# Optimization experiments

Measured on AMD Instinct MI355X. Metric: run time of the kernel, lower is better.

Reference implementation:

```python
import jax, jax.numpy as jnp
import numpy as np

B, S, E = 2, 4096, 1024
H = 16
W = 256  # attention_window == chunk size; attn width = 3*W


def _chunk3(x):
    # x: [b, nc, w, h, d] -> stack (prev, cur, next) chunks on last axis: [b, nc, w, h, d, 3]
    prev = jnp.pad(x[:, :-1], ((0, 0), (1, 0), (0, 0), (0, 0), (0, 0)))
    nxt = jnp.pad(x[:, 1:], ((0, 0), (0, 1), (0, 0), (0, 0), (0, 0)))
    return jnp.stack([prev, x, nxt], axis=-1)


def setup_inputs() -> dict:
    key = jax.random.key(0)
    ks = jax.random.split(key, 4)
    hs = jax.random.normal(ks[0], (B, S, E), jnp.float32)

    def lin(k):
        kw, kb = jax.random.split(k)
        return (jax.random.normal(kw, (E, E), jnp.float32) * 0.02,
                jax.random.normal(kb, (E,), jnp.float32) * 0.02)

    Wq, bq = lin(ks[1])
    Wk, bk = lin(ks[2])
    Wv, bv = lin(ks[3])
    return {"hidden_states": hs, "Wq": Wq, "bq": bq, "Wk": Wk, "bk": bk, "Wv": Wv, "bv": bv}


def reference(hidden_states, Wq, bq, Wk, bk, Wv, bv):
    b, s, e = hidden_states.shape
    h, w = H, W
    d = e // h
    nc = s // w  # number of non-overlapping chunks

    # torch nn.Linear: y = x @ W.T + b ; q scaled by 1/sqrt(head_dim)
    q = (hidden_states @ Wq.T + bq) * (1.0 / np.sqrt(d))
    k = hidden_states @ Wk.T + bk
    v = hidden_states @ Wv.T + bv
    q = q.reshape(b, s, h, d)
    k = k.reshape(b, s, h, d)
    v = v.reshape(b, s, h, d)

    # ---- sliding_chunks_no_overlap_matmul_qk ----
    cq = q.reshape(b, nc, w, h, d)
    ck3 = _chunk3(k.reshape(b, nc, w, h, d))  # [b,nc,w,h,d,3]
    # [b,nc,w,h,3,w] -> [b,s,h,3w]
    scores = jnp.einsum('bcxhd,bcyhde->bcxhey', cq, ck3).reshape(b, s, h, 3 * w)

    # ---- mask_invalid_locations (same math as Longformer's helper) ----
    ii = jnp.arange(w)[:, None]
    cc = jnp.arange(w + 1)[None, :]
    beg_mask = cc < (w - ii)   # [w, w+1] applied to first w rows, first w+1 cols
    end_mask = cc >= (w - ii)  # flipped mask, last w rows, last w+1 cols
    neg_inf = jnp.array(-jnp.inf, scores.dtype)
    beg = jnp.where(beg_mask[None, :, None, :], neg_inf, scores[:, :w, :, :w + 1])
    scores = scores.at[:, :w, :, :w + 1].set(beg)
    end = jnp.where(end_mask[None, :, None, :], neg_inf, scores[:, s - w:, :, 3 * w - (w + 1):])
    scores = scores.at[:, s - w:, :, 3 * w - (w + 1):].set(end)

    # softmax in float32 (as in original), cast back
    probs = jax.nn.softmax(scores.astype(jnp.float32), axis=-1).astype(hidden_states.dtype)

    # ---- sliding_chunks_no_overlap_matmul_pv ----
    cp = probs.reshape(b, nc, w, h, 3, w)          # bcwhpd (d = key pos in chunk)
    cv3 = _chunk3(v.reshape(b, nc, w, h, d))       # bcdhep (d = pos, e = head_dim, p = 3)
    attn = jnp.einsum('bcwhpd,bcdhep->bcwhe', cp, cv3).reshape(b, s, h, d)

    return attn.reshape(b, s, e)
```

## Files before the change

### kernel.cpp

```cpp
#include <hip/hip_runtime.h>
#include <math.h>

#define BB  2
#define SS  4096
#define EE  1024
#define HH  16
#define DD  64
#define WW  256
#define NCC 16
#define MTOT (BB*SS)

typedef __attribute__((ext_vector_type(4))) float f32x4;
typedef __attribute__((ext_vector_type(8))) short bf16x8;

__device__ __forceinline__ void gl_lds16(const void* g, void* l) {
  __builtin_amdgcn_global_load_lds(
      (const __attribute__((address_space(1))) unsigned int*)g,
      (__attribute__((address_space(3))) unsigned int*)l,
      16, 0, 0);
}

__device__ __forceinline__ unsigned bf16rne(float f) {
  unsigned u = __float_as_uint(f);
  return (u + (((u >> 16) & 1u) + 0x7fffu)) >> 16;
}

__device__ __forceinline__ unsigned long long pack64(unsigned a, unsigned b,
                                                     unsigned c2, unsigned d) {
  return (unsigned long long)(a | (b << 16)) |
         ((unsigned long long)(c2 | (d << 16)) << 32);
}

__global__ __launch_bounds__(256) void split_kernel(
    const float* __restrict__ x, unsigned short* __restrict__ hi,
    unsigned short* __restrict__ lo)
{
  const size_t i = (size_t)blockIdx.x * 256 + threadIdx.x;
  const float4 v = ((const float4*)x)[i];
  float f[4] = {v.x, v.y, v.z, v.w};
  unsigned short h[4], l[4];
  #pragma unroll
  for (int j = 0; j < 4; ++j) {
    unsigned u  = __float_as_uint(f[j]);
    unsigned uh = u & 0xFFFF0000u;
    h[j] = (unsigned short)(uh >> 16);
    float r = f[j] - __uint_as_float(uh);
    unsigned ur = __float_as_uint(r);
    ur += ((ur >> 16) & 1u) + 0x7FFFu;
    l[j] = (unsigned short)(ur >> 16);
  }
  *(ushort4*)&hi[4*i] = make_ushort4(h[0], h[1], h[2], h[3]);
  *(ushort4*)&lo[4*i] = make_ushort4(l[0], l[1], l[2], l[3]);
}

struct ProjArgs {
  const unsigned short* Wh;
  const unsigned short* Wl;
  const float* bias;
  unsigned short* outHi;
  unsigned short* outLo;
  float scale;
};

__global__ __launch_bounds__(256) void mfma_proj(
    const unsigned short* __restrict__ Ahi,
    const unsigned short* __restrict__ Alo,
    ProjArgs p0, ProjArgs p1, ProjArgs p2)
{
  __shared__ __align__(16) unsigned short lds[4][4096];
  const int tid  = threadIdx.x;
  const int lane = tid & 63;
  const int wid  = tid >> 6;
  const int wr   = wid >> 1, wc = wid & 1;
  const int m0   = blockIdx.x * 128, n0 = blockIdx.y * 128;
  const ProjArgs P = (blockIdx.z == 0) ? p0 : ((blockIdx.z == 1) ? p1 : p2);

  const int q0 = tid, q1 = 256 + tid;
  const int row0 = ((q0 >> 5) << 3) | (q0 & 7), kc0 = (q0 >> 3) & 3;
  const int row1 = ((q1 >> 5) << 3) | (q1 & 7), kc1 = (q1 >> 3) & 3;

  const size_t aoff0 = (size_t)(m0 + row0) * 2048 + (size_t)(kc0 * 16);
  const size_t aoff1 = (size_t)(m0 + row1) * 2048 + (size_t)(kc1 * 16);
  const size_t boff0 = (size_t)(n0 + row0) * 2048 + (size_t)(kc0 * 16);
  const size_t boff1 = (size_t)(n0 + row1) * 2048 + (size_t)(kc1 * 16);

  const int dst0 = (wid * 64) * 16;
  const int dst1 = (256 + wid * 64) * 16;

  const char* gAh = (const char*)Ahi;
  const char* gAl = (const char*)Alo;
  const char* gBh = (const char*)P.Wh;
  const char* gBl = (const char*)P.Wl;

  const int fr = lane & 15;
  const int kc = lane >> 4;
  int a_o[4], b_o[4];
  #pragma unroll
  for (int f = 0; f < 4; ++f) {
    int r = wr * 64 + f * 16 + fr;
    a_o[f] = ((r >> 3) << 9) | (kc << 7) | ((r & 7) << 4);
    r = wc * 64 + f * 16 + fr;
    b_o[f] = ((r >> 3) << 9) | (kc << 7) | ((r & 7) << 4);
  }

  f32x4 acc[4][4];
  #pragma unroll
  for (int i = 0; i < 4; ++i)
    #pragma unroll
    for (int j = 0; j < 4; ++j) acc[i][j] = (f32x4){0.f, 0.f, 0.f, 0.f};

  char* L0 = (char*)&lds[0][0];
  char* L1 = (char*)&lds[1][0];
  char* L2 = (char*)&lds[2][0];
  char* L3 = (char*)&lds[3][0];

  for (int ks = 0; ks < 32; ++ks) {
    const size_t kb = (size_t)ks * 64;
    __syncthreads();
    gl_lds16(gAh + aoff0 + kb, L0 + dst0);
    gl_lds16(gAh + aoff1 + kb, L0 + dst1);
    gl_lds16(gAl + aoff0 + kb, L1 + dst0);
    gl_lds16(gAl + aoff1 + kb, L1 + dst1);
    gl_lds16(gBh + boff0 + kb, L2 + dst0);
    gl_lds16(gBh + boff1 + kb, L2 + dst1);
    gl_lds16(gBl + boff0 + kb, L3 + dst0);
    gl_lds16(gBl + boff1 + kb, L3 + dst1);
    __syncthreads();

    bf16x8 ah[4], al[4], bh[4], bl[4];
    #pragma unroll
    for (int f = 0; f < 4; ++f) {
      ah[f] = *(const bf16x8*)(L0 + a_o[f]);
      al[f] = *(const bf16x8*)(L1 + a_o[f]);
      bh[f] = *(const bf16x8*)(L2 + b_o[f]);
      bl[f] = *(const bf16x8*)(L3 + b_o[f]);
    }
    #pragma unroll
    for (int i = 0; i < 4; ++i)
      #pragma unroll
      for (int j = 0; j < 4; ++j)
        acc[i][j] = __builtin_amdgcn_mfma_f32_16x16x32_bf16(ah[i], bh[j], acc[i][j], 0, 0, 0);
    #pragma unroll
    for (int i = 0; i < 4; ++i)
      #pragma unroll
      for (int j = 0; j < 4; ++j)
        acc[i][j] = __builtin_amdgcn_mfma_f32_16x16x32_bf16(ah[i], bl[j], acc[i][j], 0, 0, 0);
    #pragma unroll
    for (int i = 0; i < 4; ++i)
      #pragma unroll
      for (int j = 0; j < 4; ++j)
        acc[i][j] = __builtin_amdgcn_mfma_f32_16x16x32_bf16(al[i], bh[j], acc[i][j], 0, 0, 0);
  }

  const int r4 = (lane >> 4) << 2;
  #pragma unroll
  for (int j = 0; j < 4; ++j) {
    const int col = n0 + wc * 64 + j * 16 + fr;
    const float bv = P.bias[col];
    #pragma unroll
    for (int i = 0; i < 4; ++i) {
      const int rrow = m0 + wr * 64 + i * 16 + r4;
      #pragma unroll
      for (int v = 0; v < 4; ++v) {
        const float val = (acc[i][j][v] + bv) * P.scale;
        const unsigned u = __float_as_uint(val);
        const float r = val - __uint_as_float(u & 0xFFFF0000u);
        unsigned ur = __float_as_uint(r);
        ur += ((ur >> 16) & 1u) + 0x7FFFu;
        const size_t o = (size_t)(rrow + v) * EE + col;
        P.outHi[o] = (unsigned short)(u >> 16);
        P.outLo[o] = (unsigned short)(ur >> 16);
      }
    }
  }
}

__global__ __launch_bounds__(256, 2) void attn_mfma(
    const unsigned short* __restrict__ Qh_g, const unsigned short* __restrict__ Ql_g,
    const unsigned short* __restrict__ Kh_g, const unsigned short* __restrict__ Kl_g,
    const unsigned short* __restrict__ Vh_g, const unsigned short* __restrict__ Vl_g,
    float* __restrict__ Og)
{
  __shared__ __align__(16) unsigned short Kf[2][2048];
  __shared__ __align__(16) unsigned short Vt[2][2048];
  __shared__ unsigned long long Pscr[4][256];

  const int c = blockIdx.x, h = blockIdx.y, b = blockIdx.z;
  const int tid = threadIdx.x;
  const int lane = tid & 63, wid = tid >> 6;
  const int g = lane >> 4, lq = lane & 15;

  const size_t qrow0 = (size_t)(b * NCC + c) * WW;
  const int colh = h * DD;

  bf16x8 qfh[4][2], qfl[4][2];
  #pragma unroll
  for (int s = 0; s < 4; ++s)
    #pragma unroll
    for (int ch = 0; ch < 2; ++ch) {
      const size_t off = (qrow0 + wid*64 + s*16 + lq) * EE + colh + ch*32 + g*8;
      qfh[s][ch] = *(const bf16x8*)(Qh_g + off);
      qfl[s][ch] = *(const bf16x8*)(Ql_g + off);
    }

  f32x4 Oa[4][4];
  #pragma unroll
  for (int i = 0; i < 4; ++i)
    #pragma unroll
    for (int j = 0; j < 4; ++j) Oa[i][j] = (f32x4){0.f, 0.f, 0.f, 0.f};
  float m[4], lsum[4];
  #pragma unroll
  for (int s = 0; s < 4; ++s) { m[s] = -1e30f; lsum[s] = 0.f; }

  const int kK = 16*(wid & 1) + lq;
  const int dK = 32*(wid >> 1) + g*8;
  const int stv = tid >> 5, idxv = tid & 31;
  const int kV = 16*(stv >> 2) + (idxv >> 1);
  const int dV = 16*(stv & 3) + 8*(idxv & 1);
  const int C0  = ((dV >> 4) << 6) | ((kV >> 3) << 4) | (dV & 15);
  const int swW = (((dV >> 4) & 1) << 2) | (((kV >> 3) & 1) << 1) | ((dV >> 3) & 1);
  const int vel = kV & 7;

  const long krow0_base = (long)qrow0 - WW;
  const int t0 = (c == 0) ? 8 : 0;
  const int tN = (c == NCC-1) ? 16 : 24;

  uint4 rkh, rkl, rvh, rvl;
  {
    const long kr = krow0_base + (long)t0*32;
    const size_t offK = (size_t)(kr + kK) * EE + colh + dK;
    const size_t offV = (size_t)(kr + kV) * EE + colh + dV;
    rkh = *(const uint4*)(Kh_g + offK); rkl = *(const uint4*)(Kl_g + offK);
    rvh = *(const uint4*)(Vh_g + offV); rvl = *(const uint4*)(Vl_g + offV);
  }

  for (int tt = t0; tt < tN; ++tt) {
    __syncthreads();
    *(uint4*)&Kf[0][wid*512 + lane*8] = rkh;
    *(uint4*)&Kf[1][wid*512 + lane*8] = rkl;
    {
      const unsigned hw[4] = {rvh.x, rvh.y, rvh.z, rvh.w};
      const unsigned lw[4] = {rvl.x, rvl.y, rvl.z, rvl.w};
      #pragma unroll
      for (int t = 0; t < 8; ++t) {
        const int ii = C0*8 + ((t ^ swW) << 3) + vel;
        Vt[0][ii] = (unsigned short)(hw[t >> 1] >> ((t & 1) * 16));
        Vt[1][ii] = (unsigned short)(lw[t >> 1] >> ((t & 1) * 16));
      }
    }
    __syncthreads();

    if (tt + 1 < tN) {
      const long kr = krow0_base + (long)(tt+1)*32;
      const size_t offK = (size_t)(kr + kK) * EE + colh + dK;
      const size_t offV = (size_t)(kr + kV) * EE + colh + dV;
      rkh = *(const uint4*)(Kh_g + offK); rkl = *(const uint4*)(Kl_g + offK);
      rvh = *(const uint4*)(Vh_g + offV); rvl = *(const uint4*)(Vl_g + offV);
    }

    bf16x8 kfh[2][2], kfl[2][2];
    #pragma unroll
    for (int f = 0; f < 4; ++f) {
      const int o = f*512 + lane*8;
      kfh[f & 1][f >> 1] = *(const bf16x8*)&Kf[0][o];
      kfl[f & 1][f >> 1] = *(const bf16x8*)&Kf[1][o];
    }

    bf16x8 vfh[4], vfl[4];
    #pragma unroll
    for (int ds = 0; ds < 4; ++ds) {
      const int rch = ds*64 + g*16 + lq;
      const int rsw = (((rch >> 6) & 1) << 2) | (((rch >> 4) & 1) << 1) | ((rch >> 3) & 1);
      vfh[ds] = *(const bf16x8*)&Vt[0][(rch ^ rsw) * 8];
      vfl[ds] = *(const bf16x8*)&Vt[1][(rch ^ rsw) * 8];
    }

    #pragma unroll
    for (int s = 0; s < 4; ++s) {
      f32x4 ac0 = (f32x4){0.f,0.f,0.f,0.f}, ac1 = (f32x4){0.f,0.f,0.f,0.f};
      #pragma unroll
      for (int ch = 0; ch < 2; ++ch) {
        ac0 = __builtin_amdgcn_mfma_f32_16x16x32_bf16(kfh[0][ch], qfh[s][ch], ac0, 0,0,0);
        ac0 = __builtin_amdgcn_mfma_f32_16x16x32_bf16(kfh[0][ch], qfl[s][ch], ac0, 0,0,0);
        ac0 = __builtin_amdgcn_mfma_f32_16x16x32_bf16(kfl[0][ch], qfh[s][ch], ac0, 0,0,0);
        ac1 = __builtin_amdgcn_mfma_f32_16x16x32_bf16(kfh[1][ch], qfh[s][ch], ac1, 0,0,0);
        ac1 = __builtin_amdgcn_mfma_f32_16x16x32_bf16(kfh[1][ch], qfl[s][ch], ac1, 0,0,0);
        ac1 = __builtin_amdgcn_mfma_f32_16x16x32_bf16(kfl[1][ch], qfh[s][ch], ac1, 0,0,0);
      }

      float tmax = fmaxf(fmaxf(fmaxf(ac0[0],ac0[1]), fmaxf(ac0[2],ac0[3])),
                         fmaxf(fmaxf(ac1[0],ac1[1]), fmaxf(ac1[2],ac1[3])));
      tmax = fmaxf(tmax, __shfl_xor(tmax, 16));
      tmax = fmaxf(tmax, __shfl_xor(tmax, 32));
      const float mo = m[s];
      const float mn = fmaxf(mo, tmax);
      m[s] = mn;
      const float sc = __expf(mo - mn);
      float pv[8];
      #pragma unroll
      for (int r = 0; r < 4; ++r) { pv[r] = __expf(ac0[r] - mn); pv[4+r] = __expf(ac1[r] - mn); }
      float ps = 0.f;
      #pragma unroll
      for (int r = 0; r < 8; ++r) ps += pv[r];
      lsum[s] = lsum[s] * sc + ps;
      #pragma unroll
      for (int ds = 0; ds < 4; ++ds) Oa[ds][s] *= sc;

      unsigned hb[8], lb[8];
      #pragma unroll
      for (int r = 0; r < 8; ++r) {
        hb[r] = bf16rne(pv[r]);
        const float rr = pv[r] - __uint_as_float(hb[r] << 16);
        lb[r] = bf16rne(rr);
      }
      const int pq = (g >> 1)*32 + lq*2 + (g & 1);
      Pscr[wid][pq]            = pack64(hb[0],hb[1],hb[2],hb[3]);
      Pscr[wid][pq + 64]       = pack64(hb[4],hb[5],hb[6],hb[7]);
      Pscr[wid][128 + pq]      = pack64(lb[0],lb[1],lb[2],lb[3]);
      Pscr[wid][128 + pq + 64] = pack64(lb[4],lb[5],lb[6],lb[7]);
      asm volatile("" ::: "memory");
      union U8 { unsigned long long q[2]; bf16x8 v; };
      U8 uh, ul;
      uh.q[0] = Pscr[wid][lane*2];       uh.q[1] = Pscr[wid][lane*2 + 1];
      ul.q[0] = Pscr[wid][128 + lane*2]; ul.q[1] = Pscr[wid][128 + lane*2 + 1];
      const bf16x8 pbh = uh.v;
      const bf16x8 pbl = ul.v;

      #pragma unroll
      for (int ds = 0; ds < 4; ++ds) {
        Oa[ds][s] = __builtin_amdgcn_mfma_f32_16x16x32_bf16(vfh[ds], pbh, Oa[ds][s], 0,0,0);
        Oa[ds][s] = __builtin_amdgcn_mfma_f32_16x16x32_bf16(vfl[ds], pbh, Oa[ds][s], 0,0,0);
        Oa[ds][s] = __builtin_amdgcn_mfma_f32_16x16x32_bf16(vfh[ds], pbl, Oa[ds][s], 0,0,0);
      }
    }
  }

  #pragma unroll
  for (int s = 0; s < 4; ++s) {
    float ls = lsum[s];
    ls += __shfl_xor(ls, 16);
    ls += __shfl_xor(ls, 32);
    const int x = wid*64 + s*16 + lq;
    const float nz = (c == 0) ? (float)x
                   : ((c == NCC-1) ? (float)(WW - 1 - x) : 0.f);
    ls += nz * __expf(0.f - m[s]);
    const float inv = 1.f / ls;
    float* op = Og + (qrow0 + x) * EE + colh;
    #pragma unroll
    for (int ds = 0; ds < 4; ++ds) {
      float4 r;
      r.x = Oa[ds][s][0]*inv; r.y = Oa[ds][s][1]*inv;
      r.z = Oa[ds][s][2]*inv; r.w = Oa[ds][s][3]*inv;
      *(float4*)(op + ds*16 + g*4) = r;
    }
  }
}

extern "C" void kernel_launch(void* const* d_in, const int* in_sizes, int n_in,
                              void* d_out, int out_size, void* d_ws, size_t ws_size,
                              hipStream_t stream) {
    const float* hs = (const float*)d_in[0];
    const float* Wq = (const float*)d_in[1];
    const float* bq = (const float*)d_in[2];
    const float* Wk = (const float*)d_in[3];
    const float* bk = (const float*)d_in[4];
    const float* Wv = (const float*)d_in[5];
    const float* bv = (const float*)d_in[6];
    float* out = (float*)d_out;

    const size_t mat  = (size_t)MTOT * EE;
    const size_t wmat = (size_t)EE * EE;

    unsigned short* w = (unsigned short*)d_ws;
    unsigned short* Ahi = w;            unsigned short* Alo = Ahi + mat;
    unsigned short* Wqh = Alo + mat;    unsigned short* Wql = Wqh + wmat;
    unsigned short* Wkh = Wql + wmat;   unsigned short* Wkl = Wkh + wmat;
    unsigned short* Wvh = Wkl + wmat;   unsigned short* Wvl = Wvh + wmat;
    unsigned short* Qhb = Wvl + wmat;   unsigned short* Qlb = Qhb + mat;
    unsigned short* Khb = Qlb + mat;    unsigned short* Klb = Khb + mat;
    unsigned short* Vhb = Klb + mat;    unsigned short* Vlb = Vhb + mat;

    split_kernel<<<(mat/4)/256,  256, 0, stream>>>(hs, Ahi, Alo);
    split_kernel<<<(wmat/4)/256, 256, 0, stream>>>(Wq, Wqh, Wql);
    split_kernel<<<(wmat/4)/256, 256, 0, stream>>>(Wk, Wkh, Wkl);
    split_kernel<<<(wmat/4)/256, 256, 0, stream>>>(Wv, Wvh, Wvl);

    ProjArgs pq{Wqh, Wql, bq, Qhb, Qlb, 0.125f};
    ProjArgs pk{Wkh, Wkl, bk, Khb, Klb, 1.0f};
    ProjArgs pv{Wvh, Wvl, bv, Vhb, Vlb, 1.0f};
    dim3 g(MTOT/128, EE/128, 3);
    mfma_proj<<<g, 256, 0, stream>>>(Ahi, Alo, pq, pk, pv);

    dim3 ga(NCC, HH, BB);
    attn_mfma<<<ga, 256, 0, stream>>>(Qhb, Qlb, Khb, Klb, Vhb, Vlb, out);
}
```

Measured before the change: 350.4 us.

## Double-buffer LDS in projection GEMM and merge split kernels into one launch

```diff
diff --git a/kernel.cpp b/kernel.cpp
--- a/kernel.cpp
+++ b/kernel.cpp
@@ -31,12 +31,23 @@
          ((unsigned long long)(c2 | (d << 16)) << 32);
 }
 
-__global__ __launch_bounds__(256) void split_kernel(
-    const float* __restrict__ x, unsigned short* __restrict__ hi,
-    unsigned short* __restrict__ lo)
+__global__ __launch_bounds__(256) void split_all(
+    const float* __restrict__ hs, const float* __restrict__ Wq,
+    const float* __restrict__ Wk, const float* __restrict__ Wv,
+    unsigned short* __restrict__ Ahi, unsigned short* __restrict__ Alo,
+    unsigned short* __restrict__ Wqh, unsigned short* __restrict__ Wql,
+    unsigned short* __restrict__ Wkh, unsigned short* __restrict__ Wkl,
+    unsigned short* __restrict__ Wvh, unsigned short* __restrict__ Wvl)
 {
-  const size_t i = (size_t)blockIdx.x * 256 + threadIdx.x;
-  const float4 v = ((const float4*)x)[i];
+  const int bx = blockIdx.x;
+  const float* src; unsigned short *hi, *lo; size_t blk;
+  if (bx < 8192)       { src = hs; hi = Ahi; lo = Alo; blk = bx; }
+  else if (bx < 9216)  { src = Wq; hi = Wqh; lo = Wql; blk = bx - 8192; }
+  else if (bx < 10240) { src = Wk; hi = Wkh; lo = Wkl; blk = bx - 9216; }
+  else                 { src = Wv; hi = Wvh; lo = Wvl; blk = bx - 10240; }
+
+  const size_t i = blk * 256 + threadIdx.x;
+  const float4 v = ((const float4*)src)[i];
   float f[4] = {v.x, v.y, v.z, v.w};
   unsigned short h[4], l[4];
   #pragma unroll
@@ -67,7 +78,7 @@
     const unsigned short* __restrict__ Alo,
     ProjArgs p0, ProjArgs p1, ProjArgs p2)
 {
-  __shared__ __align__(16) unsigned short lds[4][4096];
+  __shared__ __align__(16) unsigned short lds[2][4][4096];
   const int tid  = threadIdx.x;
   const int lane = tid & 63;
   const int wid  = tid >> 6;
@@ -109,48 +120,57 @@
     #pragma unroll
     for (int j = 0; j < 4; ++j) acc[i][j] = (f32x4){0.f, 0.f, 0.f, 0.f};
 
-  char* L0 = (char*)&lds[0][0];
-  char* L1 = (char*)&lds[1][0];
-  char* L2 = (char*)&lds[2][0];
-  char* L3 = (char*)&lds[3][0];
-
-  for (int ks = 0; ks < 32; ++ks) {
-    const size_t kb = (size_t)ks * 64;
+  char* const Lp = (char*)&lds[0][0][0];
+  #define PL(b, p) (Lp + (((b)*4 + (p)) * 8192))
+
+  #define STAGE(buf, ks) { const size_t kb = (size_t)(ks) * 64; \
+    gl_lds16(gAh + aoff0 + kb, PL(buf,0) + dst0); \
+    gl_lds16(gAh + aoff1 + kb, PL(buf,0) + dst1); \
+    gl_lds16(gAl + aoff0 + kb, PL(buf,1) + dst0); \
+    gl_lds16(gAl + aoff1 + kb, PL(buf,1) + dst1); \
+    gl_lds16(gBh + boff0 + kb, PL(buf,2) + dst0); \
+    gl_lds16(gBh + boff1 + kb, PL(buf,2) + dst1); \
+    gl_lds16(gBl + boff0 + kb, PL(buf,3) + dst0); \
+    gl_lds16(gBl + boff1 + kb, PL(buf,3) + dst1); }
+
+  #define COMPUTE(buf) { \
+    bf16x8 ah[4], al[4], bh[4], bl[4]; \
+    _Pragma("unroll") \
+    for (int f = 0; f < 4; ++f) { \
+      ah[f] = *(const bf16x8*)(PL(buf,0) + a_o[f]); \
+      al[f] = *(const bf16x8*)(PL(buf,1) + a_o[f]); \
+      bh[f] = *(const bf16x8*)(PL(buf,2) + b_o[f]); \
+      bl[f] = *(const bf16x8*)(PL(buf,3) + b_o[f]); \
+    } \
+    _Pragma("unroll") \
+    for (int i = 0; i < 4; ++i) \
+      _Pragma("unroll") \
+      for (int j = 0; j < 4; ++j) \
+        acc[i][j] = __builtin_amdgcn_mfma_f32_16x16x32_bf16(ah[i], bh[j], acc[i][j], 0,0,0); \
+    _Pragma("unroll") \
+    for (int i = 0; i < 4; ++i) \
+      _Pragma("unroll") \
+      for (int j = 0; j < 4; ++j) \
+        acc[i][j] = __builtin_amdgcn_mfma_f32_16x16x32_bf16(ah[i], bl[j], acc[i][j], 0,0,0); \
+    _Pragma("unroll") \
+    for (int i = 0; i < 4; ++i) \
+      _Pragma("unroll") \
+      for (int j = 0; j < 4; ++j) \
+        acc[i][j] = __builtin_amdgcn_mfma_f32_16x16x32_bf16(al[i], bh[j], acc[i][j], 0,0,0); }
+
+  STAGE(0, 0);
+  __syncthreads();
+  for (int ks = 0; ks < 32; ks += 2) {
+    STAGE(1, ks + 1);
+    COMPUTE(0);
     __syncthreads();
-    gl_lds16(gAh + aoff0 + kb, L0 + dst0);
-    gl_lds16(gAh + aoff1 + kb, L0 + dst1);
-    gl_lds16(gAl + aoff0 + kb, L1 + dst0);
-    gl_lds16(gAl + aoff1 + kb, L1 + dst1);
-    gl_lds16(gBh + boff0 + kb, L2 + dst0);
-    gl_lds16(gBh + boff1 + kb, L2 + dst1);
-    gl_lds16(gBl + boff0 + kb, L3 + dst0);
-    gl_lds16(gBl + boff1 + kb, L3 + dst1);
+    if (ks + 2 < 32) STAGE(0, ks + 2);
+    COMPUTE(1);
     __syncthreads();
-
-    bf16x8 ah[4], al[4], bh[4], bl[4];
-    #pragma unroll
-    for (int f = 0; f < 4; ++f) {
-      ah[f] = *(const bf16x8*)(L0 + a_o[f]);
-      al[f] = *(const bf16x8*)(L1 + a_o[f]);
-      bh[f] = *(const bf16x8*)(L2 + b_o[f]);
-      bl[f] = *(const bf16x8*)(L3 + b_o[f]);
-    }
-    #pragma unroll
-    for (int i = 0; i < 4; ++i)
-      #pragma unroll
-      for (int j = 0; j < 4; ++j)
-        acc[i][j] = __builtin_amdgcn_mfma_f32_16x16x32_bf16(ah[i], bh[j], acc[i][j], 0, 0, 0);
-    #pragma unroll
-    for (int i = 0; i < 4; ++i)
-      #pragma unroll
-      for (int j = 0; j < 4; ++j)
-        acc[i][j] = __builtin_amdgcn_mfma_f32_16x16x32_bf16(ah[i], bl[j], acc[i][j], 0, 0, 0);
-    #pragma unroll
-    for (int i = 0; i < 4; ++i)
-      #pragma unroll
-      for (int j = 0; j < 4; ++j)
-        acc[i][j] = __builtin_amdgcn_mfma_f32_16x16x32_bf16(al[i], bh[j], acc[i][j], 0, 0, 0);
-  }
+  }
+  #undef PL
+  #undef STAGE
+  #undef COMPUTE
 
   const int r4 = (lane >> 4) << 2;
   #pragma unroll
@@ -380,10 +400,8 @@
     unsigned short* Khb = Qlb + mat;    unsigned short* Klb = Khb + mat;
     unsigned short* Vhb = Klb + mat;    unsigned short* Vlb = Vhb + mat;
 
-    split_kernel<<<(mat/4)/256,  256, 0, stream>>>(hs, Ahi, Alo);
-    split_kernel<<<(wmat/4)/256, 256, 0, stream>>>(Wq, Wqh, Wql);
-    split_kernel<<<(wmat/4)/256, 256, 0, stream>>>(Wk, Wkh, Wkl);
-    split_kernel<<<(wmat/4)/256, 256, 0, stream>>>(Wv, Wvh, Wvl);
+    split_all<<<8192 + 3*1024, 256, 0, stream>>>(
+        hs, Wq, Wk, Wv, Ahi, Alo, Wqh, Wql, Wkh, Wkl, Wvh, Wvl);
 
     ProjArgs pq{Wqh, Wql, bq, Qhb, Qlb, 0.125f};
     ProjArgs pk{Wkh, Wkl, bk, Khb, Klb, 1.0f};
```

Result: no change. 351.6 us (+0.3%).
